# Performance work log

Hardware: AMD Instinct MI355X
Metric: run time of the kernel (lower is better)

## Reference

```python
import jax, jax.numpy as jnp
import numpy as np

SCALE = 100.0

def _build_tables():
    b2n = np.zeros((256, 32), np.float32)
    n2b = np.zeros((32, 256), np.float32)
    for byte in range(256):
        h, l = byte >> 4, byte & 15
        b2n[byte, h] = 1.0
        b2n[byte, 16 + l] = 1.0
        n2b[h, byte] = 1.0
        n2b[16 + l, byte] = 1.0
    add_table = np.zeros((16, 16, 2, 16), np.float32)
    carry_table = np.zeros((16, 16, 2, 2), np.float32)
    for x in range(16):
        for y in range(16):
            for c in range(2):
                t = x + y + c
                add_table[x, y, c, t % 16] = 1.0
                carry_table[x, y, c, t // 16] = 1.0
    return b2n, n2b, add_table, carry_table

def setup_inputs() -> dict:
    key = jax.random.key(0)
    k1, k2 = jax.random.split(key)
    B = 32768
    a = jax.random.normal(k1, (B, 4, 256), dtype=jnp.float32)
    b = jax.random.normal(k2, (B, 4, 256), dtype=jnp.float32)
    b2n, n2b, add_table, carry_table = _build_tables()
    return {"a": a, "b": b,
            "b2n": jnp.asarray(b2n), "n2b": jnp.asarray(n2b),
            "add_table": jnp.asarray(add_table), "carry_table": jnp.asarray(carry_table)}

def _byte_add_single(a, b, b2n, n2b, add_table, carry_table):
    # a, b: [4, 256]
    def to_nibbles(x):
        comb = x @ b2n  # [32]
        return jax.nn.softmax(comb[:16] * SCALE), jax.nn.softmax(comb[16:] * SCALE)

    def nibble_add(x, y, cin):
        # cin has shape [1] initially (broadcasts over carry axis, as torch einsum does) or [2]
        w = x[:, None, None] * y[None, :, None] * cin[None, None, :]
        w = jnp.broadcast_to(w, (16, 16, 2))
        s = jnp.einsum('ijk,ijkl->l', w, add_table)
        c = jnp.einsum('ijk,ijkl->l', w, carry_table)
        return jax.nn.softmax(s * SCALE), jax.nn.softmax(c * SCALE)

    def from_nibbles(h, l):
        return jax.nn.softmax((jnp.concatenate([h, l]) @ n2b) * SCALE)

    carry = jnp.ones((1,), a.dtype)  # matches torch.tensor([1.0]) initial carry
    outs = []
    for i in range(4):  # fixed 4-byte carry chain
        ah, al = to_nibbles(a[i])
        bh, bl = to_nibbles(b[i])
        sl, carry_out = nibble_add(al, bl, carry)
        sh, carry = nibble_add(ah, bh, carry_out)
        outs.append(from_nibbles(sh, sl))
    return jnp.stack(outs)  # [4, 256]

def reference(a, b, b2n, n2b, add_table, carry_table):
    f = jax.vmap(_byte_add_single, in_axes=(0, 0, None, None, None, None))
    return f(a, b, b2n, n2b, add_table, carry_table)  # [B, 4, 256]
```

## Files before the change

### kernel.cpp

```cpp
#include <hip/hip_runtime.h>
#include <cstddef>
#include <math.h>


__device__ __forceinline__ float exf(float t) {
  return (float)exp((double)t);
}

__device__ __forceinline__ void softmax16_np(const float* comb, float* p) {
#pragma clang fp contract(off)
  float t[16];
#pragma unroll
  for (int j = 0; j < 16; ++j) t[j] = comb[j] * 100.0f;
  float m = t[0];
#pragma unroll
  for (int j = 1; j < 16; ++j) m = fmaxf(m, t[j]);
  float e[16];
#pragma unroll
  for (int j = 0; j < 16; ++j) e[j] = exf(t[j] - m);
  float r0 = e[0] + e[8], r1 = e[1] + e[9], r2 = e[2] + e[10], r3 = e[3] + e[11];
  float r4 = e[4] + e[12], r5 = e[5] + e[13], r6 = e[6] + e[14], r7 = e[7] + e[15];
  float s = ((r0 + r1) + (r2 + r3)) + ((r4 + r5) + (r6 + r7));
#pragma unroll
  for (int j = 0; j < 16; ++j) p[j] = e[j] / s;
}

__device__ __forceinline__ void nibble_add_np(const float* px, const float* py,
                                              float c0, float c1,
                                              float* ps, float& n0, float& n1) {
#pragma clang fp contract(off)
  float s[16];
  float ca = 0.f, cb = 0.f;
#pragma unroll
  for (int l = 0; l < 16; ++l) s[l] = 0.f;
#pragma unroll
  for (int i = 0; i < 16; ++i) {
#pragma unroll
    for (int j = 0; j < 16; ++j) {
      float wij = px[i] * py[j];
      float w0 = wij * c0;
      float w1 = wij * c1;
      const int t0 = i + j, t1 = i + j + 1;
      s[t0 & 15] += w0;
      if (t0 < 16) ca += w0; else cb += w0;
      s[t1 & 15] += w1;
      if (t1 < 16) ca += w1; else cb += w1;
    }
  }
  softmax16_np(s, ps);
  float t0 = ca * 100.0f, t1 = cb * 100.0f;
  float m = fmaxf(t0, t1);
  float e0 = exf(t0 - m), e1 = exf(t1 - m);
  float ss = e0 + e1;
  n0 = e0 / ss;
  n1 = e1 / ss;
}

__device__ __forceinline__ void buckets_np(const float* __restrict__ row,
                                           float* hi, float* lo) {
#pragma clang fp contract(off)
#pragma unroll
  for (int j = 0; j < 16; ++j) { hi[j] = 0.f; lo[j] = 0.f; }
#pragma unroll
  for (int k4 = 0; k4 < 64; ++k4) {
    float4 x = *(const float4*)(row + k4 * 4);
    const int h = k4 >> 2, l0 = (k4 & 3) * 4;
    hi[h] += x.x;  hi[h] += x.y;  hi[h] += x.z;  hi[h] += x.w;
    lo[l0 + 0] += x.x;
    lo[l0 + 1] += x.y;
    lo[l0 + 2] += x.z;
    lo[l0 + 3] += x.w;
  }
}

extern "C" __global__ void __launch_bounds__(64, 1)
byteadd_kernel(const float* __restrict__ A, const float* __restrict__ Bm,
               float* __restrict__ O, int nbatch) {
#pragma clang fp contract(off)
  const int b = blockIdx.x * 64 + threadIdx.x;
  if (b >= nbatch) return;
  const float* Ab = A + (size_t)b * 1024;
  const float* Bb = Bm + (size_t)b * 1024;
  float* Ob = O + (size_t)b * 1024;

  float cr0 = 1.0f, cr1 = 1.0f;

#pragma unroll 1
  for (int i = 0; i < 4; ++i) {
    float ah[16], al[16], bh[16], bl[16];
    buckets_np(Ab + i * 256, ah, al);
    buckets_np(Bb + i * 256, bh, bl);
    float pah[16], pal[16], pbh[16], pbl[16];
    softmax16_np(ah, pah);
    softmax16_np(al, pal);
    softmax16_np(bh, pbh);
    softmax16_np(bl, pbl);

    float psl[16], psh[16], d0, d1;
    nibble_add_np(pal, pbl, cr0, cr1, psl, d0, d1);
    nibble_add_np(pah, pbh, d0, d1, psh, cr0, cr1);

    float ph2[16], pl2[16];
    softmax16_np(psh, ph2);
    softmax16_np(psl, pl2);

#pragma unroll
    for (int k4 = 0; k4 < 64; ++k4) {
      const int h = k4 >> 2, l0 = (k4 & 3) * 4;
      const float ph = ph2[h];
      float4 o;
      o.x = ph * pl2[l0 + 0];
      o.y = ph * pl2[l0 + 1];
      o.z = ph * pl2[l0 + 2];
      o.w = ph * pl2[l0 + 3];
      *(float4*)(Ob + i * 256 + k4 * 4) = o;
    }
  }
}

extern "C" void kernel_launch(void* const* d_in, const int* in_sizes, int n_in,
                              void* d_out, int out_size, void* d_ws, size_t ws_size,
                              hipStream_t stream) {
  const float* A = (const float*)d_in[0];
  const float* B = (const float*)d_in[1];
  float* O = (float*)d_out;
  int nbatch = in_sizes[0] / 1024;
  int blocks = (nbatch + 63) / 64;
  byteadd_kernel<<<dim3(blocks), dim3(64), 0, stream>>>(A, B, O, nbatch);
}
```

Measured before the change: 192.5 us.

## Stage rows through shared memory with 256-thread blocks and cooperative bucketing

Each block now uses 256 threads for 64 batch elements instead of one thread per batch element. Input rows are loaded with coalesced float4 reads into LDS, nibble bucket sums are split across 8 threads per row, and softmaxes are spread across threads. Output is written through LDS with coalesced stores. The aim is to replace strided per-thread row accesses and the low occupancy of 64-thread blocks, at the cost of many __syncthreads and a serial carry-chain phase where only 64 threads are active.

```diff
diff --git a/kernel.cpp b/kernel.cpp
--- a/kernel.cpp
+++ b/kernel.cpp
@@ -7,11 +7,11 @@
   return (float)exp((double)t);
 }
 
-__device__ __forceinline__ void softmax16_np(const float* comb, float* p) {
+__device__ __forceinline__ void softmax16_np(const float* x, float* p) {
 #pragma clang fp contract(off)
   float t[16];
 #pragma unroll
-  for (int j = 0; j < 16; ++j) t[j] = comb[j] * 100.0f;
+  for (int j = 0; j < 16; ++j) t[j] = x[j] * 100.0f;
   float m = t[0];
 #pragma unroll
   for (int j = 1; j < 16; ++j) m = fmaxf(m, t[j]);
@@ -25,11 +25,10 @@
   for (int j = 0; j < 16; ++j) p[j] = e[j] / s;
 }
 
-__device__ __forceinline__ void nibble_add_np(const float* px, const float* py,
-                                              float c0, float c1,
-                                              float* ps, float& n0, float& n1) {
+__device__ __forceinline__ void nibble_add_raw(const float* px, const float* py,
+                                               float c0, float c1,
+                                               float* s, float& n0, float& n1) {
 #pragma clang fp contract(off)
-  float s[16];
   float ca = 0.f, cb = 0.f;
 #pragma unroll
   for (int l = 0; l < 16; ++l) s[l] = 0.f;
@@ -47,73 +46,129 @@
       if (t1 < 16) ca += w1; else cb += w1;
     }
   }
-  softmax16_np(s, ps);
-  float t0 = ca * 100.0f, t1 = cb * 100.0f;
-  float m = fmaxf(t0, t1);
-  float e0 = exf(t0 - m), e1 = exf(t1 - m);
+  float u0 = ca * 100.0f, u1 = cb * 100.0f;
+  float m = fmaxf(u0, u1);
+  float e0 = exf(u0 - m), e1 = exf(u1 - m);
   float ss = e0 + e1;
   n0 = e0 / ss;
   n1 = e1 / ss;
 }
 
-__device__ __forceinline__ void buckets_np(const float* __restrict__ row,
-                                           float* hi, float* lo) {
-#pragma clang fp contract(off)
-#pragma unroll
-  for (int j = 0; j < 16; ++j) { hi[j] = 0.f; lo[j] = 0.f; }
-#pragma unroll
-  for (int k4 = 0; k4 < 64; ++k4) {
-    float4 x = *(const float4*)(row + k4 * 4);
-    const int h = k4 >> 2, l0 = (k4 & 3) * 4;
-    hi[h] += x.x;  hi[h] += x.y;  hi[h] += x.z;  hi[h] += x.w;
-    lo[l0 + 0] += x.x;
-    lo[l0 + 1] += x.y;
-    lo[l0 + 2] += x.z;
-    lo[l0 + 3] += x.w;
-  }
-}
-
-extern "C" __global__ void __launch_bounds__(64, 1)
+extern "C" __global__ void __launch_bounds__(256, 2)
 byteadd_kernel(const float* __restrict__ A, const float* __restrict__ Bm,
                float* __restrict__ O, int nbatch) {
-#pragma clang fp contract(off)
-  const int b = blockIdx.x * 64 + threadIdx.x;
-  if (b >= nbatch) return;
-  const float* Ab = A + (size_t)b * 1024;
-  const float* Bb = Bm + (size_t)b * 1024;
-  float* Ob = O + (size_t)b * 1024;
+  __shared__ float buf[32][260];
+  __shared__ float comb[64][67];
+  __shared__ float pout[64][36];
+
+  const int tid = threadIdx.x;
+  const int batch0 = blockIdx.x * 64;
+  if (batch0 >= nbatch) return;
 
   float cr0 = 1.0f, cr1 = 1.0f;
 
 #pragma unroll 1
   for (int i = 0; i < 4; ++i) {
-    float ah[16], al[16], bh[16], bl[16];
-    buckets_np(Ab + i * 256, ah, al);
-    buckets_np(Bb + i * 256, bh, bl);
-    float pah[16], pal[16], pbh[16], pbl[16];
-    softmax16_np(ah, pah);
-    softmax16_np(al, pal);
-    softmax16_np(bh, pbh);
-    softmax16_np(bl, pbl);
+    for (int inp = 0; inp < 2; ++inp) {
+      const float* __restrict__ src = (inp == 0) ? A : Bm;
+      for (int h = 0; h < 2; ++h) {
+        __syncthreads();
+#pragma unroll
+        for (int r = 0; r < 8; ++r) {
+          int row = r * 4 + (tid >> 6);
+          int c4 = tid & 63;
+          const float* p = src + ((size_t)(batch0 + h * 32 + row) * 1024 + i * 256 + c4 * 4);
+          *(float4*)&buf[row][c4 * 4] = *(const float4*)p;
+        }
+        __syncthreads();
+        {
+#pragma clang fp contract(off)
+          int bb = tid >> 3;
+          int g = tid & 7;
+          float acc[4] = {0.f, 0.f, 0.f, 0.f};
+          if (g < 4) {
+#pragma unroll
+            for (int u4 = 0; u4 < 4; ++u4)
+#pragma unroll
+              for (int k4 = 0; k4 < 4; ++k4) {
+                float4 v = *(const float4*)&buf[bb][g * 64 + u4 * 16 + k4 * 4];
+                acc[u4] += v.x; acc[u4] += v.y; acc[u4] += v.z; acc[u4] += v.w;
+              }
+#pragma unroll
+            for (int u4 = 0; u4 < 4; ++u4)
+              comb[h * 32 + bb][inp * 34 + g * 4 + u4] = acc[u4];
+          } else {
+            int l0 = (g - 4) * 4;
+#pragma unroll
+            for (int k = 0; k < 16; ++k) {
+              float4 v = *(const float4*)&buf[bb][l0 + k * 16];
+              acc[0] += v.x; acc[1] += v.y; acc[2] += v.z; acc[3] += v.w;
+            }
+#pragma unroll
+            for (int q = 0; q < 4; ++q)
+              comb[h * 32 + bb][inp * 34 + 16 + l0 + q] = acc[q];
+          }
+        }
+      }
+    }
+    __syncthreads();
 
-    float psl[16], psh[16], d0, d1;
-    nibble_add_np(pal, pbl, cr0, cr1, psl, d0, d1);
-    nibble_add_np(pah, pbh, d0, d1, psh, cr0, cr1);
+    {
+      int bb = tid >> 2, w = tid & 3;
+      int off = (w >> 1) * 34 + (w & 1) * 16;
+      float x[16], p[16];
+#pragma unroll
+      for (int j = 0; j < 16; ++j) x[j] = comb[bb][off + j];
+      softmax16_np(x, p);
+#pragma unroll
+      for (int j = 0; j < 16; ++j) comb[bb][off + j] = p[j];
+    }
+    __syncthreads();
 
-    float ph2[16], pl2[16];
-    softmax16_np(psh, ph2);
-    softmax16_np(psl, pl2);
+    if (tid < 64) {
+      float pxl[16], pyl[16];
+#pragma unroll
+      for (int j = 0; j < 16; ++j) { pxl[j] = comb[tid][16 + j]; pyl[j] = comb[tid][50 + j]; }
+      float sl[16], d0, d1;
+      nibble_add_raw(pxl, pyl, cr0, cr1, sl, d0, d1);
+#pragma unroll
+      for (int j = 0; j < 16; ++j) pout[tid][20 + j] = sl[j];
+      float pxh[16], pyh[16];
+#pragma unroll
+      for (int j = 0; j < 16; ++j) { pxh[j] = comb[tid][j]; pyh[j] = comb[tid][34 + j]; }
+      float sh[16];
+      nibble_add_raw(pxh, pyh, d0, d1, sh, cr0, cr1);
+#pragma unroll
+      for (int j = 0; j < 16; ++j) pout[tid][j] = sh[j];
+    }
+    __syncthreads();
+
+    if (tid < 128) {
+      int bb = tid >> 1;
+      int off = (tid & 1) * 20;
+      float x[16], p[16], p2[16];
+#pragma unroll
+      for (int j = 0; j < 16; ++j) x[j] = pout[bb][off + j];
+      softmax16_np(x, p);
+      softmax16_np(p, p2);
+#pragma unroll
+      for (int j = 0; j < 16; ++j) pout[bb][off + j] = p2[j];
+    }
+    __syncthreads();
 
 #pragma unroll
-    for (int k4 = 0; k4 < 64; ++k4) {
-      const int h = k4 >> 2, l0 = (k4 & 3) * 4;
-      const float ph = ph2[h];
+    for (int kk = 0; kk < 16; ++kk) {
+      int flat = kk * 1024 + tid * 4;
+      int bb = flat >> 8;
+      int b0 = flat & 255;
+      float ph = pout[bb][b0 >> 4];
+      int lo = 20 + (b0 & 15);
       float4 o;
-      o.x = ph * pl2[l0 + 0];
-      o.y = ph * pl2[l0 + 1];
-      o.z = ph * pl2[l0 + 2];
-      o.w = ph * pl2[l0 + 3];
-      *(float4*)(Ob + i * 256 + k4 * 4) = o;
+      o.x = ph * pout[bb][lo + 0];
+      o.y = ph * pout[bb][lo + 1];
+      o.z = ph * pout[bb][lo + 2];
+      o.w = ph * pout[bb][lo + 3];
+      *(float4*)(O + ((size_t)(batch0 + bb) * 4 + i) * 256 + b0) = o;
     }
   }
 }
@@ -126,5 +181,5 @@
   float* O = (float*)d_out;
   int nbatch = in_sizes[0] / 1024;
   int blocks = (nbatch + 63) / 64;
-  byteadd_kernel<<<dim3(blocks), dim3(64), 0, stream>>>(A, B, O, nbatch);
+  byteadd_kernel<<<dim3(blocks), dim3(256), 0, stream>>>(A, B, O, nbatch);
 }
```

Measured after the change: 238.8 us. 1.24x slower.

## Split byte-add into three kernels: prep, carry chain, output expansion

Applied to the files above, without the earlier changes.

Replaces the single thread-per-batch kernel with three launches. The first stages inputs through shared memory and writes nibble softmaxes to a workspace in batch-major-transposed layout. The second runs only the serial carry chain with coalesced workspace reads. The third applies the final softmaxes and writes the 256-wide outputs cooperatively. The aim is better parallelism and coalesced memory access than the original one-thread-per-row design, which used strided per-thread loads and low occupancy. The cost is extra workspace traffic and two more launches, and it falls back to the old kernel when the workspace is too small.

```diff
diff --git a/kernel.cpp b/kernel.cpp
--- a/kernel.cpp
+++ b/kernel.cpp
@@ -7,11 +7,11 @@
   return (float)exp((double)t);
 }
 
-__device__ __forceinline__ void softmax16_np(const float* comb, float* p) {
+__device__ __forceinline__ void softmax16_np(const float* x, float* p) {
 #pragma clang fp contract(off)
   float t[16];
 #pragma unroll
-  for (int j = 0; j < 16; ++j) t[j] = comb[j] * 100.0f;
+  for (int j = 0; j < 16; ++j) t[j] = x[j] * 100.0f;
   float m = t[0];
 #pragma unroll
   for (int j = 1; j < 16; ++j) m = fmaxf(m, t[j]);
@@ -25,11 +25,10 @@
   for (int j = 0; j < 16; ++j) p[j] = e[j] / s;
 }
 
-__device__ __forceinline__ void nibble_add_np(const float* px, const float* py,
-                                              float c0, float c1,
-                                              float* ps, float& n0, float& n1) {
-#pragma clang fp contract(off)
-  float s[16];
+__device__ __forceinline__ void nibble_add_raw(const float* px, const float* py,
+                                               float c0, float c1,
+                                               float* s, float& n0, float& n1) {
+#pragma clang fp contract(off)
   float ca = 0.f, cb = 0.f;
 #pragma unroll
   for (int l = 0; l < 16; ++l) s[l] = 0.f;
@@ -47,17 +46,161 @@
       if (t1 < 16) ca += w1; else cb += w1;
     }
   }
-  softmax16_np(s, ps);
-  float t0 = ca * 100.0f, t1 = cb * 100.0f;
-  float m = fmaxf(t0, t1);
-  float e0 = exf(t0 - m), e1 = exf(t1 - m);
+  float u0 = ca * 100.0f, u1 = cb * 100.0f;
+  float m = fmaxf(u0, u1);
+  float e0 = exf(u0 - m), e1 = exf(u1 - m);
   float ss = e0 + e1;
   n0 = e0 / ss;
   n1 = e1 / ss;
 }
 
-__device__ __forceinline__ void buckets_np(const float* __restrict__ row,
-                                           float* hi, float* lo) {
+extern "C" __global__ void __launch_bounds__(256, 1)
+k1_prep(const float* __restrict__ A, const float* __restrict__ Bm,
+        float* __restrict__ ws1, int nbatch) {
+  __shared__ float buf[32][257];
+  __shared__ float comb[32][33];
+  const int tid = threadIdx.x;
+  const int batch0 = blockIdx.x * 32;
+  const int ib = blockIdx.y;
+  const int inp = blockIdx.z;
+  if (batch0 >= nbatch) return;
+  const float* __restrict__ src =
+      (inp == 0 ? A : Bm) + (size_t)batch0 * 1024 + ib * 256;
+
+#pragma unroll
+  for (int r = 0; r < 8; ++r) {
+    int idx = r * 256 + tid;
+    int row = idx >> 6, c4 = idx & 63;
+    *(float4*)&buf[row][c4 * 4] = *(const float4*)(src + (size_t)row * 1024 + c4 * 4);
+  }
+  __syncthreads();
+
+  {
+#pragma clang fp contract(off)
+    const int g = tid >> 5, bb = tid & 31;
+    float acc[4] = {0.f, 0.f, 0.f, 0.f};
+    if (g < 4) {
+#pragma unroll
+      for (int q = 0; q < 4; ++q) {
+        float a = 0.f;
+#pragma unroll
+        for (int k4 = 0; k4 < 4; ++k4) {
+          float4 v = *(const float4*)&buf[bb][(g * 4 + q) * 16 + k4 * 4];
+          a += v.x; a += v.y; a += v.z; a += v.w;
+        }
+        acc[q] = a;
+      }
+#pragma unroll
+      for (int q = 0; q < 4; ++q) comb[bb][g * 4 + q] = acc[q];
+    } else {
+      const int l0 = (g - 4) * 4;
+#pragma unroll
+      for (int m = 0; m < 16; ++m) {
+        float4 v = *(const float4*)&buf[bb][m * 16 + l0];
+        acc[0] += v.x; acc[1] += v.y; acc[2] += v.z; acc[3] += v.w;
+      }
+#pragma unroll
+      for (int q = 0; q < 4; ++q) comb[bb][16 + l0 + q] = acc[q];
+    }
+  }
+  __syncthreads();
+
+  if (tid < 64) {
+    const int nib = tid >> 5, bb = tid & 31;
+    float x[16], p[16];
+#pragma unroll
+    for (int j = 0; j < 16; ++j) x[j] = comb[bb][nib * 16 + j];
+    softmax16_np(x, p);
+    const size_t r0 = (size_t)((ib * 2 + inp) * 32 + nib * 16);
+#pragma unroll
+    for (int j = 0; j < 16; ++j)
+      ws1[(r0 + j) * nbatch + batch0 + bb] = p[j];
+  }
+}
+
+__device__ __forceinline__ void k2_load(const float* __restrict__ ws1, int i,
+                                        size_t batch, int nbatch, float* b) {
+#pragma unroll
+  for (int t = 0; t < 64; ++t)
+    b[t] = ws1[(size_t)(i * 64 + t) * nbatch + batch];
+}
+
+__device__ __forceinline__ void k2_step(const float* b, float& cr0, float& cr1,
+                                        float* __restrict__ ws2, int i,
+                                        size_t batch, int nbatch) {
+  float sl[16], sh[16], d0, d1;
+  nibble_add_raw(b + 16, b + 48, cr0, cr1, sl, d0, d1);
+  nibble_add_raw(b + 0,  b + 32, d0, d1, sh, cr0, cr1);
+#pragma unroll
+  for (int l = 0; l < 16; ++l) {
+    ws2[(size_t)(i * 32 + l) * nbatch + batch] = sh[l];
+    ws2[(size_t)(i * 32 + 16 + l) * nbatch + batch] = sl[l];
+  }
+}
+
+extern "C" __global__ void __launch_bounds__(64, 1)
+k2_chain(const float* __restrict__ ws1, float* __restrict__ ws2, int nbatch) {
+  const size_t batch = (size_t)blockIdx.x * 64 + threadIdx.x;
+  if (batch >= (size_t)nbatch) return;
+  float cr0 = 1.0f, cr1 = 1.0f;
+  float bufA[64], bufB[64];
+  k2_load(ws1, 0, batch, nbatch, bufA);
+  k2_load(ws1, 1, batch, nbatch, bufB);
+  k2_step(bufA, cr0, cr1, ws2, 0, batch, nbatch);
+  k2_load(ws1, 2, batch, nbatch, bufA);
+  k2_step(bufB, cr0, cr1, ws2, 1, batch, nbatch);
+  k2_load(ws1, 3, batch, nbatch, bufB);
+  k2_step(bufA, cr0, cr1, ws2, 2, batch, nbatch);
+  k2_step(bufB, cr0, cr1, ws2, 3, batch, nbatch);
+}
+
+extern "C" __global__ void __launch_bounds__(256, 1)
+k3_out(const float* __restrict__ ws2, float* __restrict__ O, int nbatch) {
+  __shared__ float pout[64][36];
+  const int tid = threadIdx.x;
+  const int batch0 = blockIdx.x * 64;
+  const int ib = blockIdx.y;
+  if (batch0 >= nbatch) return;
+
+  if (tid < 128) {
+    const int nib = tid >> 6, bb = tid & 63;
+    float x[16], p[16], p2[16];
+#pragma unroll
+    for (int l = 0; l < 16; ++l)
+      x[l] = ws2[(size_t)(ib * 32 + nib * 16 + l) * nbatch + batch0 + bb];
+    softmax16_np(x, p);
+    softmax16_np(p, p2);
+#pragma unroll
+    for (int j = 0; j < 16; ++j) pout[bb][nib * 20 + j] = p2[j];
+  }
+  __syncthreads();
+
+#pragma unroll
+  for (int kk = 0; kk < 16; ++kk) {
+    int flat = kk * 1024 + tid * 4;
+    int bb = flat >> 8;
+    int b0 = flat & 255;
+    float ph = pout[bb][b0 >> 4];
+    int lo = 20 + (b0 & 15);
+    float4 o;
+    o.x = ph * pout[bb][lo + 0];
+    o.y = ph * pout[bb][lo + 1];
+    o.z = ph * pout[bb][lo + 2];
+    o.w = ph * pout[bb][lo + 3];
+    *(float4*)(O + ((size_t)(batch0 + bb) * 4 + ib) * 256 + b0) = o;
+  }
+}
+
+__device__ __forceinline__ void nibble_add_np_fb(const float* px, const float* py,
+                                                 float c0, float c1,
+                                                 float* ps, float& n0, float& n1) {
+  float s[16];
+  nibble_add_raw(px, py, c0, c1, s, n0, n1);
+  softmax16_np(s, ps);
+}
+
+__device__ __forceinline__ void buckets_np_fb(const float* __restrict__ row,
+                                              float* hi, float* lo) {
 #pragma clang fp contract(off)
 #pragma unroll
   for (int j = 0; j < 16; ++j) { hi[j] = 0.f; lo[j] = 0.f; }
@@ -74,36 +217,31 @@
 }
 
 extern "C" __global__ void __launch_bounds__(64, 1)
-byteadd_kernel(const float* __restrict__ A, const float* __restrict__ Bm,
-               float* __restrict__ O, int nbatch) {
+byteadd_fallback(const float* __restrict__ A, const float* __restrict__ Bm,
+                 float* __restrict__ O, int nbatch) {
 #pragma clang fp contract(off)
   const int b = blockIdx.x * 64 + threadIdx.x;
   if (b >= nbatch) return;
   const float* Ab = A + (size_t)b * 1024;
   const float* Bb = Bm + (size_t)b * 1024;
   float* Ob = O + (size_t)b * 1024;
-
   float cr0 = 1.0f, cr1 = 1.0f;
-
 #pragma unroll 1
   for (int i = 0; i < 4; ++i) {
     float ah[16], al[16], bh[16], bl[16];
-    buckets_np(Ab + i * 256, ah, al);
-    buckets_np(Bb + i * 256, bh, bl);
+    buckets_np_fb(Ab + i * 256, ah, al);
+    buckets_np_fb(Bb + i * 256, bh, bl);
     float pah[16], pal[16], pbh[16], pbl[16];
     softmax16_np(ah, pah);
     softmax16_np(al, pal);
     softmax16_np(bh, pbh);
     softmax16_np(bl, pbl);
-
     float psl[16], psh[16], d0, d1;
-    nibble_add_np(pal, pbl, cr0, cr1, psl, d0, d1);
-    nibble_add_np(pah, pbh, d0, d1, psh, cr0, cr1);
-
+    nibble_add_np_fb(pal, pbl, cr0, cr1, psl, d0, d1);
+    nibble_add_np_fb(pah, pbh, d0, d1, psh, cr0, cr1);
     float ph2[16], pl2[16];
     softmax16_np(psh, ph2);
     softmax16_np(psl, pl2);
-
 #pragma unroll
     for (int k4 = 0; k4 < 64; ++k4) {
       const int h = k4 >> 2, l0 = (k4 & 3) * 4;
@@ -125,6 +263,14 @@
   const float* B = (const float*)d_in[1];
   float* O = (float*)d_out;
   int nbatch = in_sizes[0] / 1024;
-  int blocks = (nbatch + 63) / 64;
-  byteadd_kernel<<<dim3(blocks), dim3(64), 0, stream>>>(A, B, O, nbatch);
-}
+  size_t need = (size_t)384 * nbatch * sizeof(float);
+  if (ws_size >= need && (nbatch & 63) == 0) {
+    float* ws1 = (float*)d_ws;
+    float* ws2 = ws1 + (size_t)256 * nbatch;
+    k1_prep<<<dim3(nbatch / 32, 4, 2), dim3(256), 0, stream>>>(A, B, ws1, nbatch);
+    k2_chain<<<dim3(nbatch / 64), dim3(64), 0, stream>>>(ws1, ws2, nbatch);
+    k3_out<<<dim3(nbatch / 64, 4), dim3(256), 0, stream>>>(ws2, O, nbatch);
+  } else {
+    byteadd_fallback<<<dim3((nbatch + 63) / 64), dim3(64), 0, stream>>>(A, B, O, nbatch);
+  }
+}
```

After: 197.1 us. 2.4% more time.
